# Kernel optimization log

Hardware: AMD Instinct MI355X
Metric: run time of the kernel (lower is better)

The kernel has to match this reference:

```python
import jax, jax.numpy as jnp
import numpy as np

GRID_SIZE = 8
POS_LAMBDA = 250.0
POS_MARGIN = 1.0
NEG_MARGIN = 0.2


def setup_inputs() -> dict:
    key = jax.random.key(0)
    k1, k2, k3, k4 = jax.random.split(key, 4)
    N, C, Hr, Wr = 8, 128, 30, 40
    H, W = Hr * GRID_SIZE, Wr * GRID_SIZE
    des1 = jax.random.normal(k1, (N, C, Hr, Wr), jnp.float32)
    des2 = jax.random.normal(k2, (N, C, Hr, Wr), jnp.float32)
    # near-identity homography so the positive-pair mask s is non-trivial
    homo = jnp.eye(3, dtype=jnp.float32) + 0.001 * jax.random.normal(k3, (3, 3), jnp.float32)
    mask = (jax.random.uniform(k4, (N, 1, H, W)) > 0.05).astype(jnp.float32)
    return {"des1": des1, "des2": des2, "homo": homo, "mask": mask}


def reference(des1, des2, homo, mask):
    n, c, hr, wr = des1.shape
    gs = GRID_SIZE

    # coordinate grid of cell centers in full-res pixel coords: (x, y)
    ys, xs = jnp.meshgrid(jnp.arange(hr), jnp.arange(wr), indexing='ij')
    grid = jnp.stack([xs, ys], axis=-1).astype(homo.dtype) * gs + gs // 2  # Hr,Wr,2
    grid = jnp.broadcast_to(grid, (n, hr, wr, 2))

    # warp grid by homography
    gh = jnp.concatenate([grid, jnp.ones((n, hr, wr, 1), homo.dtype)], axis=-1)  # N,Hr,Wr,3
    wg = jnp.einsum('nhwk,jk->nhwj', gh, homo)
    w_grid = wg[..., :2] / wg[..., 2:3]  # N,Hr,Wr,2

    # pairwise distance between grid cells of img1 and warped cells of img2
    diff = grid[:, :, :, None, None, :] - w_grid[:, None, None, :, :, :]  # N,Hr,Wr,Hr,Wr,2
    grid_dist = jnp.sqrt(jnp.sum(diff * diff, axis=-1))                   # N,Hr,Wr,Hr,Wr
    s = (grid_dist <= gs - 0.5).astype(des1.dtype)

    # dense descriptor cross-correlation (contraction over channels)
    dot_des = jnp.einsum('ncij,nckl->nijkl', des1, des2)  # N,Hr,Wr,Hr,Wr

    pos_dist = jnp.maximum(POS_MARGIN - dot_des, 0.0)
    neg_dist = jnp.maximum(dot_des - NEG_MARGIN, 0.0)
    loss = POS_LAMBDA * s * pos_dist + (1.0 - s) * neg_dist

    # space_to_depth(mask, gs).prod(dim=1)
    m = mask.reshape(n, 1, hr, gs, wr, gs)
    r_mask = jnp.prod(m, axis=(1, 3, 5))            # N,Hr,Wr
    r_mask5 = r_mask.reshape(n, 1, 1, hr, wr)

    norm = hr * wr * jnp.sum(r_mask5)
    loss = jnp.sum(loss * r_mask5) / norm
    return (loss, s, dot_des, r_mask5[:, 0])  # r_mask squeezed -> N,1,Hr,Wr
```

## Files before the change

### kernel.cpp

```cpp
#include <hip/hip_runtime.h>
#include <hip/hip_bf16.h>

#define HRr 30
#define WRr 40
#define MM 1200
#define CC 128
#define NB 8
#define GS 8

constexpr int PT = 19;
constexpr int TILE_SH = 16 * 64 * 8;
constexpr int NPART = 1200;

typedef __attribute__((ext_vector_type(8))) short bf16x8;
typedef __attribute__((ext_vector_type(4))) float f32x4;

__device__ inline short f2bf(float f) {
    union { float f; unsigned u; } v; v.f = f;
    unsigned r = v.u + 0x7FFFu + ((v.u >> 16) & 1u);
    return (short)(r >> 16);
}

__global__ __launch_bounds__(256) void convert_prep_kernel(const float* __restrict__ des1,
                                                           const float* __restrict__ des2,
                                                           const float* __restrict__ homo,
                                                           const float* __restrict__ mask,
                                                           short* __restrict__ wsA,
                                                           short* __restrict__ wsB,
                                                           float2* __restrict__ wgrid,
                                                           float* __restrict__ out_rmask,
                                                           float* __restrict__ ws_rmask) {
    const int t     = threadIdx.x;
    const int ptile = blockIdx.x;
    const int n     = blockIdx.z;

    if (blockIdx.y == 0) {
        const int gid = (blockIdx.z * gridDim.x + blockIdx.x) * 256 + t;
        if (gid < MM) {
            int k = gid / WRr, l = gid % WRr;
            float x = (float)(l * GS + GS / 2);
            float y = (float)(k * GS + GS / 2);
            float nx = homo[0] * x + homo[1] * y + homo[2];
            float ny = homo[3] * x + homo[4] * y + homo[5];
            float dn = homo[6] * x + homo[7] * y + homo[8];
            wgrid[gid] = make_float2(nx / dn, ny / dn);
        }
        if (gid < NB * MM) {
            int nn = gid / MM;
            int rem = gid % MM;
            int k = rem / WRr, l = rem % WRr;
            const float* mp = mask + (size_t)nn * (240 * 320) + (size_t)(k * GS) * 320 + l * GS;
            float prod = 1.f;
            #pragma unroll
            for (int yy = 0; yy < GS; ++yy) {
                float4 a = *reinterpret_cast<const float4*>(&mp[yy * 320]);
                float4 b = *reinterpret_cast<const float4*>(&mp[yy * 320 + 4]);
                prod *= a.x * a.y * a.z * a.w * b.x * b.y * b.z * b.w;
            }
            out_rmask[gid] = prod;
            ws_rmask[gid]  = prod;
        }
    }

    const int j = t & 63;
    const int g = t >> 6;
    const int p = ptile * 64 + j;

    const float* A = des1 + (size_t)n * CC * MM;
    const float* B = des2 + (size_t)n * CC * MM;
    short* outA = wsA + (size_t)(n * PT + ptile) * TILE_SH;
    short* outB = wsB + (size_t)(n * PT + ptile) * TILE_SH;

    const int rb = j >> 4, lc = j & 15;
    const int kr = blockIdx.y * 4 + g;
    const int kb = kr * 8;
    bf16x8 wa, wb;
    #pragma unroll
    for (int i = 0; i < 8; ++i) {
        float va = (p < MM) ? A[(size_t)(kb + i) * MM + p] : 0.f;
        float vb = (p < MM) ? B[(size_t)(kb + i) * MM + p] : 0.f;
        wa[i] = f2bf(va);
        wb[i] = f2bf(vb);
    }
    const int ks = kr >> 2, lr = kr & 3;
    const size_t off = (size_t)(((ks * 4 + rb) * 64) + lr * 16 + lc) * 8;
    *reinterpret_cast<bf16x8*>(&outA[off]) = wa;
    *reinterpret_cast<bf16x8*>(&outB[off]) = wb;
}

__global__ __launch_bounds__(256) void main_kernel(const short* __restrict__ wsA,
                                                   const short* __restrict__ wsB,
                                                   const float2* __restrict__ wgrid,
                                                   const float* __restrict__ rmask,
                                                   float* __restrict__ out_s,
                                                   float* __restrict__ out_dot,
                                                   float* __restrict__ partials) {
    __shared__ float Ds[16 * 612];
    __shared__ float red[4];

    const int f   = blockIdx.x;
    const int lid = (f & 7) * 150 + (f >> 3);
    const int n     = lid / 150;
    const int rem   = lid % 150;
    const int strip = rem >> 1;
    const int half  = rem & 1;
    const int p0    = strip * 16;
    const int cbase = half ? 608 : 0;
    const int nf    = half ? 37  : 38;
    const int W     = half ? 592 : 608;
    const int fbase = half ? 38  : 0;

    const int t    = threadIdx.x;
    const int lane = t & 63;
    const int w    = t >> 6;
    const int lr   = lane >> 4, lc = lane & 15;

    const short* An  = wsA + (size_t)(n * PT + (p0 >> 6)) * TILE_SH;
    const int    rbA = (p0 >> 4) & 3;
    bf16x8 af[4];
    #pragma unroll
    for (int ks = 0; ks < 4; ++ks)
        af[ks] = *reinterpret_cast<const bf16x8*>(&An[(size_t)(((ks * 4 + rbA) * 64) + lane) * 8]);

    const short* Bn = wsB + (size_t)n * PT * TILE_SH;
    const float* rm = rmask + n * MM;

    auto do_frag = [&](int i) {
        const int g = fbase + i;
        const short* Bt = Bn + (size_t)(g >> 2) * TILE_SH;
        const int rbB = g & 3;
        f32x4 acc = {0.f, 0.f, 0.f, 0.f};
        #pragma unroll
        for (int ks = 0; ks < 4; ++ks) {
            bf16x8 bfr = *reinterpret_cast<const bf16x8*>(
                &Bt[(size_t)(((ks * 4 + rbB) * 64) + lane) * 8]);
            acc = __builtin_amdgcn_mfma_f32_16x16x32_bf16(af[ks], bfr, acc, 0, 0, 0);
        }
        #pragma unroll
        for (int r = 0; r < 4; ++r)
            Ds[(lr * 4 + r) * 612 + 1 + i * 16 + lc] = acc[r];
    };

    const int row = t >> 4;
    const int l16 = t & 15;
    const int p   = p0 + row;
    const float gx = (float)((p % WRr) * GS + GS / 2);
    const float gy = (float)((p / WRr) * GS + GS / 2);
    const size_t rowbase = (size_t)(n * MM + p) * MM;
    const int h = 31 - 16 * (p & 1);

    float lsum = 0.f;

    auto emit_scalar = [&](int c) {
        const float dot = Ds[row * 612 + 1 + c];
        const int q = cbase + c;
        const float2 wg = wgrid[q];
        const float dx = gx - wg.x, dy = gy - wg.y;
        const float dist = sqrtf(dx * dx + dy * dy);
        const float s = (dist <= 7.5f) ? 1.f : 0.f;
        const float le = 250.f * s * fmaxf(1.f - dot, 0.f) + (1.f - s) * fmaxf(dot - 0.2f, 0.f);
        lsum += le * rm[q];
        __builtin_nontemporal_store(dot, &out_dot[rowbase + q]);
        __builtin_nontemporal_store(s, &out_s[rowbase + q]);
    };

    auto emit_range = [&](int cLo, int cHi) {
        int cAl = cLo + (((h - cLo) % 32) + 32) % 32;
        if (cAl > cHi) cAl = cHi;
        for (int c = cLo + l16; c < cAl; c += 16) emit_scalar(c);
        const int nl = (cHi - cAl) >> 5;
        const int s4 = nl << 3;
        const int cTs = cAl + (nl << 5);
        for (int k = 0;; ++k) {
            const int jj = l16 + (k << 4);
            if (jj >= s4) break;
            const int c = cAl + (jj << 2);
            const int q = cbase + c;
            const f32x4 dv = *reinterpret_cast<const f32x4*>(&Ds[row * 612 + 1 + c]);
            f32x4 sv;
            #pragma unroll
            for (int u = 0; u < 4; ++u) {
                const float2 wg = wgrid[q + u];
                const float dx = gx - wg.x, dy = gy - wg.y;
                const float dist = sqrtf(dx * dx + dy * dy);
                const float s = (dist <= 7.5f) ? 1.f : 0.f;
                sv[u] = s;
                const float le = 250.f * s * fmaxf(1.f - dv[u], 0.f) + (1.f - s) * fmaxf(dv[u] - 0.2f, 0.f);
                lsum += le * rm[q + u];
            }
            __builtin_nontemporal_store(dv, reinterpret_cast<f32x4*>(&out_dot[rowbase + q]));
            __builtin_nontemporal_store(sv, reinterpret_cast<f32x4*>(&out_s[rowbase + q]));
        }
        for (int c = cTs + l16; c < cHi; c += 16) emit_scalar(c);
    };

    for (int i = w; i < 20; i += 4) do_frag(i);
    __syncthreads();

    for (int i = 20 + w; i < nf; i += 4) do_frag(i);
    const int c_split = h + 288;
    emit_range(0, c_split);
    __syncthreads();

    emit_range(c_split, W);

    #pragma unroll
    for (int off = 32; off > 0; off >>= 1)
        lsum += __shfl_xor(lsum, off, 64);
    if (lane == 0) red[w] = lsum;
    __syncthreads();
    if (t == 0)
        partials[lid] = (red[0] + red[1]) + (red[2] + red[3]);
}

__global__ __launch_bounds__(1024) void final_kernel(const float* __restrict__ partials,
                                                     const float* __restrict__ rmask,
                                                     float* __restrict__ out_loss) {
    __shared__ float r1[16], r2[16];
    const int t = threadIdx.x;
    const int lane = t & 63;
    const int w = t >> 6;

    float s1 = 0.f, s2 = 0.f;
    for (int i = t; i < NPART; i += 1024) s1 += partials[i];
    for (int i = t; i < NB * MM; i += 1024) s2 += rmask[i];
    #pragma unroll
    for (int off = 32; off > 0; off >>= 1) {
        s1 += __shfl_xor(s1, off, 64);
        s2 += __shfl_xor(s2, off, 64);
    }
    if (lane == 0) { r1[w] = s1; r2[w] = s2; }
    __syncthreads();
    if (t == 0) {
        float total = 0.f, rsum = 0.f;
        #pragma unroll
        for (int i = 0; i < 16; ++i) { total += r1[i]; rsum += r2[i]; }
        out_loss[0] = total / ((float)MM * rsum);
    }
}

extern "C" void kernel_launch(void* const* d_in, const int* in_sizes, int n_in,
                              void* d_out, int out_size, void* d_ws, size_t ws_size,
                              hipStream_t stream) {
    const float* des1 = (const float*)d_in[0];
    const float* des2 = (const float*)d_in[1];
    const float* homo = (const float*)d_in[2];
    const float* mask = (const float*)d_in[3];

    float* out      = (float*)d_out;
    float* out_loss = out;
    float* out_s    = out + 1;
    float* out_dot  = out + 1 + (size_t)NB * MM * MM;
    float* out_rm   = out + 1 + 2 * (size_t)NB * MM * MM;

    char* wsb = (char*)d_ws;
    float2* wgrid    = (float2*)(wsb);
    float*  partials = (float*)(wsb + 16384);
    float*  ws_rm    = (float*)(wsb + 32768);
    short*  wsA      = (short*)(wsb + 131072);
    short*  wsB      = wsA + (size_t)NB * PT * TILE_SH;

    dim3 cgrid(PT, 4, NB);
    convert_prep_kernel<<<cgrid, 256, 0, stream>>>(des1, des2, homo, mask,
                                                   wsA, wsB, wgrid, out_rm, ws_rm);

    main_kernel<<<dim3(NPART, 1, 1), 256, 0, stream>>>(wsA, wsB, wgrid, ws_rm,
                                                       out_s, out_dot, partials);

    final_kernel<<<1, 1024, 0, stream>>>(partials, ws_rm, out_loss);
}
```

Baseline: 48.33 us.

## Warp-specialize MFMA and store phases, fold final reduction into last block

In the second phase, two waves finish the remaining MFMA fragments while the other two waves already emit the first column region for all 16 rows. Afterwards every wave writes the second region for its own four rows. The separate final reduction kernel is removed: an atomic counter lets the last finishing block sum the partials and the mask total, which saves a launch. Stores also switch from nontemporal to plain stores, which may change cache behaviour for the large output writes.

Result: slower. 90.98 us (+88.3%).

```diff
diff --git a/kernel.cpp b/kernel.cpp
--- a/kernel.cpp
+++ b/kernel.cpp
@@ -29,10 +29,14 @@
                                                            short* __restrict__ wsB,
                                                            float2* __restrict__ wgrid,
                                                            float* __restrict__ out_rmask,
-                                                           float* __restrict__ ws_rmask) {
+                                                           float* __restrict__ ws_rmask,
+                                                           int* __restrict__ counter) {
     const int t     = threadIdx.x;
     const int ptile = blockIdx.x;
     const int n     = blockIdx.z;
+
+    if (blockIdx.x == 0 && blockIdx.y == 0 && blockIdx.z == 0 && t == 0)
+        *counter = 0;
 
     if (blockIdx.y == 0) {
         const int gid = (blockIdx.z * gridDim.x + blockIdx.x) * 256 + t;
@@ -94,9 +98,12 @@
                                                    const float* __restrict__ rmask,
                                                    float* __restrict__ out_s,
                                                    float* __restrict__ out_dot,
-                                                   float* __restrict__ partials) {
+                                                   float* __restrict__ partials,
+                                                   int* __restrict__ counter,
+                                                   float* __restrict__ out_loss) {
     __shared__ float Ds[16 * 612];
-    __shared__ float red[4];
+    __shared__ float red[4], red2[4];
+    __shared__ int lastFlag;
 
     const int f   = blockIdx.x;
     const int lid = (f & 7) * 150 + (f >> 3);
@@ -114,6 +121,7 @@
     const int lane = t & 63;
     const int w    = t >> 6;
     const int lr   = lane >> 4, lc = lane & 15;
+    const int l16  = lane & 15;
 
     const short* An  = wsA + (size_t)(n * PT + (p0 >> 6)) * TILE_SH;
     const int    rbA = (p0 >> 4) & 3;
@@ -141,17 +149,9 @@
             Ds[(lr * 4 + r) * 612 + 1 + i * 16 + lc] = acc[r];
     };
 
-    const int row = t >> 4;
-    const int l16 = t & 15;
-    const int p   = p0 + row;
-    const float gx = (float)((p % WRr) * GS + GS / 2);
-    const float gy = (float)((p / WRr) * GS + GS / 2);
-    const size_t rowbase = (size_t)(n * MM + p) * MM;
-    const int h = 31 - 16 * (p & 1);
-
     float lsum = 0.f;
 
-    auto emit_scalar = [&](int c) {
+    auto emit_scalar = [&](int row, int c, size_t rowbase, float gx, float gy) {
         const float dot = Ds[row * 612 + 1 + c];
         const int q = cbase + c;
         const float2 wg = wgrid[q];
@@ -160,82 +160,103 @@
         const float s = (dist <= 7.5f) ? 1.f : 0.f;
         const float le = 250.f * s * fmaxf(1.f - dot, 0.f) + (1.f - s) * fmaxf(dot - 0.2f, 0.f);
         lsum += le * rm[q];
-        __builtin_nontemporal_store(dot, &out_dot[rowbase + q]);
-        __builtin_nontemporal_store(s, &out_s[rowbase + q]);
-    };
-
-    auto emit_range = [&](int cLo, int cHi) {
-        int cAl = cLo + (((h - cLo) % 32) + 32) % 32;
-        if (cAl > cHi) cAl = cHi;
-        for (int c = cLo + l16; c < cAl; c += 16) emit_scalar(c);
-        const int nl = (cHi - cAl) >> 5;
+        out_dot[rowbase + q] = dot;
+        out_s[rowbase + q] = s;
+    };
+
+    auto emit_f4 = [&](int row, int c, size_t rowbase, float gx, float gy) {
+        const int q = cbase + c;
+        const f32x4 dv = *reinterpret_cast<const f32x4*>(&Ds[row * 612 + 1 + c]);
+        f32x4 sv;
+        #pragma unroll
+        for (int u = 0; u < 4; ++u) {
+            const float2 wg = wgrid[q + u];
+            const float dx = gx - wg.x, dy = gy - wg.y;
+            const float dist = sqrtf(dx * dx + dy * dy);
+            const float s = (dist <= 7.5f) ? 1.f : 0.f;
+            sv[u] = s;
+            const float le = 250.f * s * fmaxf(1.f - dv[u], 0.f) + (1.f - s) * fmaxf(dv[u] - 0.2f, 0.f);
+            lsum += le * rm[q + u];
+        }
+        *reinterpret_cast<f32x4*>(&out_dot[rowbase + q]) = dv;
+        *reinterpret_cast<f32x4*>(&out_s[rowbase + q]) = sv;
+    };
+
+    auto writeRegion1 = [&](int row) {
+        const int p = p0 + row;
+        const float gx = (float)((p % WRr) * GS + GS / 2);
+        const float gy = (float)((p / WRr) * GS + GS / 2);
+        const size_t rowbase = (size_t)(n * MM + p) * MM;
+        const int h = 31 - 16 * (p & 1);
+        for (int c = l16; c < h; c += 16) emit_scalar(row, c, rowbase, gx, gy);
+        for (int k = 0;; ++k) {
+            const int jj = l16 + (k << 4);
+            if (jj >= 72) break;
+            emit_f4(row, h + (jj << 2), rowbase, gx, gy);
+        }
+    };
+
+    auto writeRegion2 = [&](int row) {
+        const int p = p0 + row;
+        const float gx = (float)((p % WRr) * GS + GS / 2);
+        const float gy = (float)((p / WRr) * GS + GS / 2);
+        const size_t rowbase = (size_t)(n * MM + p) * MM;
+        const int h = 31 - 16 * (p & 1);
+        const int c0 = h + 288;
+        const int nl = (W - c0) >> 5;
         const int s4 = nl << 3;
-        const int cTs = cAl + (nl << 5);
+        const int ts = c0 + (nl << 5);
         for (int k = 0;; ++k) {
             const int jj = l16 + (k << 4);
             if (jj >= s4) break;
-            const int c = cAl + (jj << 2);
-            const int q = cbase + c;
-            const f32x4 dv = *reinterpret_cast<const f32x4*>(&Ds[row * 612 + 1 + c]);
-            f32x4 sv;
-            #pragma unroll
-            for (int u = 0; u < 4; ++u) {
-                const float2 wg = wgrid[q + u];
-                const float dx = gx - wg.x, dy = gy - wg.y;
-                const float dist = sqrtf(dx * dx + dy * dy);
-                const float s = (dist <= 7.5f) ? 1.f : 0.f;
-                sv[u] = s;
-                const float le = 250.f * s * fmaxf(1.f - dv[u], 0.f) + (1.f - s) * fmaxf(dv[u] - 0.2f, 0.f);
-                lsum += le * rm[q + u];
-            }
-            __builtin_nontemporal_store(dv, reinterpret_cast<f32x4*>(&out_dot[rowbase + q]));
-            __builtin_nontemporal_store(sv, reinterpret_cast<f32x4*>(&out_s[rowbase + q]));
-        }
-        for (int c = cTs + l16; c < cHi; c += 16) emit_scalar(c);
+            emit_f4(row, c0 + (jj << 2), rowbase, gx, gy);
+        }
+        for (int c = ts + l16; c < W; c += 16) emit_scalar(row, c, rowbase, gx, gy);
     };
 
     for (int i = w; i < 20; i += 4) do_frag(i);
     __syncthreads();
 
-    for (int i = 20 + w; i < nf; i += 4) do_frag(i);
-    const int c_split = h + 288;
-    emit_range(0, c_split);
-    __syncthreads();
-
-    emit_range(c_split, W);
+    if (w < 2) {
+        for (int i = 20 + w; i < nf; i += 2) do_frag(i);
+    } else {
+        const int r0 = (w - 2) * 8 + (lane >> 4);
+        writeRegion1(r0);
+        writeRegion1(r0 + 4);
+    }
+    __syncthreads();
+
+    writeRegion2(w * 4 + (lane >> 4));
 
     #pragma unroll
     for (int off = 32; off > 0; off >>= 1)
         lsum += __shfl_xor(lsum, off, 64);
     if (lane == 0) red[w] = lsum;
     __syncthreads();
-    if (t == 0)
+    if (t == 0) {
         partials[lid] = (red[0] + red[1]) + (red[2] + red[3]);
-}
-
-__global__ __launch_bounds__(1024) void final_kernel(const float* __restrict__ partials,
-                                                     const float* __restrict__ rmask,
-                                                     float* __restrict__ out_loss) {
-    __shared__ float r1[16], r2[16];
-    const int t = threadIdx.x;
-    const int lane = t & 63;
-    const int w = t >> 6;
-
-    float s1 = 0.f, s2 = 0.f;
-    for (int i = t; i < NPART; i += 1024) s1 += partials[i];
-    for (int i = t; i < NB * MM; i += 1024) s2 += rmask[i];
-    #pragma unroll
-    for (int off = 32; off > 0; off >>= 1) {
-        s1 += __shfl_xor(s1, off, 64);
-        s2 += __shfl_xor(s2, off, 64);
-    }
-    if (lane == 0) { r1[w] = s1; r2[w] = s2; }
-    __syncthreads();
-    if (t == 0) {
-        float total = 0.f, rsum = 0.f;
-        #pragma unroll
-        for (int i = 0; i < 16; ++i) { total += r1[i]; rsum += r2[i]; }
-        out_loss[0] = total / ((float)MM * rsum);
+        __threadfence();
+        const int old = atomicAdd(counter, 1);
+        lastFlag = (old == NPART - 1) ? 1 : 0;
+    }
+    __syncthreads();
+
+    if (lastFlag) {
+        float s1 = 0.f, s2 = 0.f;
+        for (int i = t; i < NPART; i += 256) s1 += partials[i];
+        for (int i = t; i < NB * MM; i += 256) s2 += rmask[i];
+        #pragma unroll
+        for (int off = 32; off > 0; off >>= 1) {
+            s1 += __shfl_xor(s1, off, 64);
+            s2 += __shfl_xor(s2, off, 64);
+        }
+        if (lane == 0) { red[w] = s1; red2[w] = s2; }
+        __syncthreads();
+        if (t == 0) {
+            const float total = (red[0] + red[1]) + (red[2] + red[3]);
+            const float rsum  = (red2[0] + red2[1]) + (red2[2] + red2[3]);
+            out_loss[0] = total / ((float)MM * rsum);
+        }
     }
 }
 
@@ -256,16 +277,16 @@
     char* wsb = (char*)d_ws;
     float2* wgrid    = (float2*)(wsb);
     float*  partials = (float*)(wsb + 16384);
+    int*    counter  = (int*)(wsb + 24576);
     float*  ws_rm    = (float*)(wsb + 32768);
     short*  wsA      = (short*)(wsb + 131072);
     short*  wsB      = wsA + (size_t)NB * PT * TILE_SH;
 
     dim3 cgrid(PT, 4, NB);
     convert_prep_kernel<<<cgrid, 256, 0, stream>>>(des1, des2, homo, mask,
-                                                   wsA, wsB, wgrid, out_rm, ws_rm);
+                                                   wsA, wsB, wgrid, out_rm, ws_rm, counter);
 
     main_kernel<<<dim3(NPART, 1, 1), 256, 0, stream>>>(wsA, wsB, wgrid, ws_rm,
-                                                       out_s, out_dot, partials);
-
-    final_kernel<<<1, 1024, 0, stream>>>(partials, ws_rm, out_loss);
-}
+                                                       out_s, out_dot, partials,
+                                                       counter, out_loss);
+}
```

## Split main kernel into quarter-column blocks and simplify convert kernel work split

Applied to the files above, without the earlier changes.

The main kernel now gives each 16-row strip four blocks of about 304 columns instead of two of about 608. This halves shared memory per block and doubles the grid to 2400 blocks for more occupancy. The intra-block overlap of MFMA fragments with emission is dropped in favour of one sync, and nontemporal stores become plain stores. The convert kernel now has each wave handle either des1 or des2, doubling the grid in y. These changes trade the overlap and the streaming-store hint for more parallelism, and may add cache pollution on the large output writes.

After: 40.16 us. 1.2x faster.

```diff
diff --git a/kernel.cpp b/kernel.cpp
--- a/kernel.cpp
+++ b/kernel.cpp
@@ -10,7 +10,7 @@
 
 constexpr int PT = 19;
 constexpr int TILE_SH = 16 * 64 * 8;
-constexpr int NPART = 1200;
+constexpr int NPART = 2400;
 
 typedef __attribute__((ext_vector_type(8))) short bf16x8;
 typedef __attribute__((ext_vector_type(4))) float f32x4;
@@ -62,30 +62,26 @@
         }
     }
 
-    const int j = t & 63;
-    const int g = t >> 6;
-    const int p = ptile * 64 + j;
-
-    const float* A = des1 + (size_t)n * CC * MM;
-    const float* B = des2 + (size_t)n * CC * MM;
-    short* outA = wsA + (size_t)(n * PT + ptile) * TILE_SH;
-    short* outB = wsB + (size_t)(n * PT + ptile) * TILE_SH;
-
-    const int rb = j >> 4, lc = j & 15;
-    const int kr = blockIdx.y * 4 + g;
-    const int kb = kr * 8;
-    bf16x8 wa, wb;
+    const int lane = t & 63;
+    const int g    = t >> 6;
+    const int p    = ptile * 64 + lane;
+    const int kr   = blockIdx.y * 2 + (g >> 1);
+    const int kb   = kr * 8;
+    const int isB  = g & 1;
+
+    const float* src = (isB ? des2 : des1) + (size_t)n * CC * MM;
+    short* dst = (isB ? wsB : wsA) + (size_t)(n * PT + ptile) * TILE_SH;
+
+    bf16x8 wv;
     #pragma unroll
     for (int i = 0; i < 8; ++i) {
-        float va = (p < MM) ? A[(size_t)(kb + i) * MM + p] : 0.f;
-        float vb = (p < MM) ? B[(size_t)(kb + i) * MM + p] : 0.f;
-        wa[i] = f2bf(va);
-        wb[i] = f2bf(vb);
-    }
-    const int ks = kr >> 2, lr = kr & 3;
-    const size_t off = (size_t)(((ks * 4 + rb) * 64) + lr * 16 + lc) * 8;
-    *reinterpret_cast<bf16x8*>(&outA[off]) = wa;
-    *reinterpret_cast<bf16x8*>(&outB[off]) = wb;
+        float v = (p < MM) ? src[(size_t)(kb + i) * MM + p] : 0.f;
+        wv[i] = f2bf(v);
+    }
+    const int rb = lane >> 4, lc = lane & 15;
+    const int ks = kr >> 2, lrk = kr & 3;
+    const size_t off = (size_t)(((ks * 4 + rb) * 64) + lrk * 16 + lc) * 8;
+    *reinterpret_cast<bf16x8*>(&dst[off]) = wv;
 }
 
 __global__ __launch_bounds__(256) void main_kernel(const short* __restrict__ wsA,
@@ -95,20 +91,20 @@
                                                    float* __restrict__ out_s,
                                                    float* __restrict__ out_dot,
                                                    float* __restrict__ partials) {
-    __shared__ float Ds[16 * 612];
+    __shared__ float Ds[16 * 308];
     __shared__ float red[4];
 
     const int f   = blockIdx.x;
-    const int lid = (f & 7) * 150 + (f >> 3);
-    const int n     = lid / 150;
-    const int rem   = lid % 150;
-    const int strip = rem >> 1;
-    const int half  = rem & 1;
+    const int lid = (f & 7) * 300 + (f >> 3);
+    const int n       = lid / 300;
+    const int rem     = lid % 300;
+    const int strip   = rem >> 2;
+    const int quarter = rem & 3;
     const int p0    = strip * 16;
-    const int cbase = half ? 608 : 0;
-    const int nf    = half ? 37  : 38;
-    const int W     = half ? 592 : 608;
-    const int fbase = half ? 38  : 0;
+    const int cbase = quarter * 304;
+    const int nf    = (quarter < 3) ? 19 : 18;
+    const int W     = (quarter < 3) ? 304 : 288;
+    const int fbase = quarter * 19;
 
     const int t    = threadIdx.x;
     const int lane = t & 63;
@@ -125,7 +121,7 @@
     const short* Bn = wsB + (size_t)n * PT * TILE_SH;
     const float* rm = rmask + n * MM;
 
-    auto do_frag = [&](int i) {
+    for (int i = w; i < nf; i += 4) {
         const int g = fbase + i;
         const short* Bt = Bn + (size_t)(g >> 2) * TILE_SH;
         const int rbB = g & 3;
@@ -138,8 +134,9 @@
         }
         #pragma unroll
         for (int r = 0; r < 4; ++r)
-            Ds[(lr * 4 + r) * 612 + 1 + i * 16 + lc] = acc[r];
-    };
+            Ds[(lr * 4 + r) * 308 + 1 + i * 16 + lc] = acc[r];
+    }
+    __syncthreads();
 
     const int row = t >> 4;
     const int l16 = t & 15;
@@ -148,11 +145,12 @@
     const float gy = (float)((p / WRr) * GS + GS / 2);
     const size_t rowbase = (size_t)(n * MM + p) * MM;
     const int h = 31 - 16 * (p & 1);
+    const int cAl = (((h - cbase) % 32) + 32) % 32;
 
     float lsum = 0.f;
 
-    auto emit_scalar = [&](int c) {
-        const float dot = Ds[row * 612 + 1 + c];
+    for (int c = l16; c < cAl; c += 16) {
+        const float dot = Ds[row * 308 + 1 + c];
         const int q = cbase + c;
         const float2 wg = wgrid[q];
         const float dx = gx - wg.x, dy = gy - wg.y;
@@ -160,49 +158,44 @@
         const float s = (dist <= 7.5f) ? 1.f : 0.f;
         const float le = 250.f * s * fmaxf(1.f - dot, 0.f) + (1.f - s) * fmaxf(dot - 0.2f, 0.f);
         lsum += le * rm[q];
-        __builtin_nontemporal_store(dot, &out_dot[rowbase + q]);
-        __builtin_nontemporal_store(s, &out_s[rowbase + q]);
-    };
-
-    auto emit_range = [&](int cLo, int cHi) {
-        int cAl = cLo + (((h - cLo) % 32) + 32) % 32;
-        if (cAl > cHi) cAl = cHi;
-        for (int c = cLo + l16; c < cAl; c += 16) emit_scalar(c);
-        const int nl = (cHi - cAl) >> 5;
-        const int s4 = nl << 3;
-        const int cTs = cAl + (nl << 5);
-        for (int k = 0;; ++k) {
-            const int jj = l16 + (k << 4);
-            if (jj >= s4) break;
-            const int c = cAl + (jj << 2);
-            const int q = cbase + c;
-            const f32x4 dv = *reinterpret_cast<const f32x4*>(&Ds[row * 612 + 1 + c]);
-            f32x4 sv;
-            #pragma unroll
-            for (int u = 0; u < 4; ++u) {
-                const float2 wg = wgrid[q + u];
-                const float dx = gx - wg.x, dy = gy - wg.y;
-                const float dist = sqrtf(dx * dx + dy * dy);
-                const float s = (dist <= 7.5f) ? 1.f : 0.f;
-                sv[u] = s;
-                const float le = 250.f * s * fmaxf(1.f - dv[u], 0.f) + (1.f - s) * fmaxf(dv[u] - 0.2f, 0.f);
-                lsum += le * rm[q + u];
-            }
-            __builtin_nontemporal_store(dv, reinterpret_cast<f32x4*>(&out_dot[rowbase + q]));
-            __builtin_nontemporal_store(sv, reinterpret_cast<f32x4*>(&out_s[rowbase + q]));
-        }
-        for (int c = cTs + l16; c < cHi; c += 16) emit_scalar(c);
-    };
-
-    for (int i = w; i < 20; i += 4) do_frag(i);
-    __syncthreads();
-
-    for (int i = 20 + w; i < nf; i += 4) do_frag(i);
-    const int c_split = h + 288;
-    emit_range(0, c_split);
-    __syncthreads();
-
-    emit_range(c_split, W);
+        out_dot[rowbase + q] = dot;
+        out_s[rowbase + q] = s;
+    }
+    const int nl = (W - cAl) >> 5;
+    const int s4 = nl << 3;
+    const int ts = cAl + (nl << 5);
+    for (int k = 0;; ++k) {
+        const int jj = l16 + (k << 4);
+        if (jj >= s4) break;
+        const int c = cAl + (jj << 2);
+        const int q = cbase + c;
+        const f32x4 dv = *reinterpret_cast<const f32x4*>(&Ds[row * 308 + 1 + c]);
+        f32x4 sv;
+        #pragma unroll
+        for (int u = 0; u < 4; ++u) {
+            const float2 wg = wgrid[q + u];
+            const float dx = gx - wg.x, dy = gy - wg.y;
+            const float dist = sqrtf(dx * dx + dy * dy);
+            const float s = (dist <= 7.5f) ? 1.f : 0.f;
+            sv[u] = s;
+            const float le = 250.f * s * fmaxf(1.f - dv[u], 0.f) + (1.f - s) * fmaxf(dv[u] - 0.2f, 0.f);
+            lsum += le * rm[q + u];
+        }
+        *reinterpret_cast<f32x4*>(&out_dot[rowbase + q]) = dv;
+        *reinterpret_cast<f32x4*>(&out_s[rowbase + q]) = sv;
+    }
+    for (int c = ts + l16; c < W; c += 16) {
+        const float dot = Ds[row * 308 + 1 + c];
+        const int q = cbase + c;
+        const float2 wg = wgrid[q];
+        const float dx = gx - wg.x, dy = gy - wg.y;
+        const float dist = sqrtf(dx * dx + dy * dy);
+        const float s = (dist <= 7.5f) ? 1.f : 0.f;
+        const float le = 250.f * s * fmaxf(1.f - dot, 0.f) + (1.f - s) * fmaxf(dot - 0.2f, 0.f);
+        lsum += le * rm[q];
+        out_dot[rowbase + q] = dot;
+        out_s[rowbase + q] = s;
+    }
 
     #pragma unroll
     for (int off = 32; off > 0; off >>= 1)
@@ -260,7 +253,7 @@
     short*  wsA      = (short*)(wsb + 131072);
     short*  wsB      = wsA + (size_t)NB * PT * TILE_SH;
 
-    dim3 cgrid(PT, 4, NB);
+    dim3 cgrid(PT, 8, NB);
     convert_prep_kernel<<<cgrid, 256, 0, stream>>>(des1, des2, homo, mask,
                                                    wsA, wsB, wgrid, out_rm, ws_rm);
 
```
